# Performance work log

Measured on AMD Instinct MI355X. Metric: run time of the kernel, lower is better.

The kernel has to match this reference:

```python
import jax, jax.numpy as jnp
import numpy as np

KSIZE = 3
KN = (KSIZE - 1) // 2  # 1
TEMP = 50.0


def _extract_patches(x, same_pad):
    """TF tf.image.extract_patches ordering: per location, (dy, dx, channel).
    x: [b,H,W,d] -> [b,h,w,9*d] (h=H,w=W if same_pad else H-2,W-2)."""
    if same_pad:
        x = jnp.pad(x, ((0, 0), (KN, KN), (KN, KN), (0, 0)))
    b, Hp, Wp, d = x.shape
    h, w = Hp - 2 * KN, Wp - 2 * KN
    slices = [x[:, dy:dy + h, dx:dx + w, :]
              for dy in range(KSIZE) for dx in range(KSIZE)]
    return jnp.concatenate(slices, axis=-1)


def setup_inputs() -> dict:
    key = jax.random.key(0)
    k1, k2, k3 = jax.random.split(key, 3)
    b, h, w, dims = 4, 48, 48, 64
    g_in = jax.random.normal(k1, (b, h, w, dims), dtype=jnp.float32)
    # binary inpainting mask (1 = known background, 0 = hole)
    mask = (jax.random.uniform(k2, (b, h, w, 1)) > 0.5).astype(jnp.float32)
    W2 = jax.random.normal(k3, (2 * dims, dims), dtype=jnp.float32) / np.sqrt(2.0 * dims)
    b2 = jnp.zeros((dims,), dtype=jnp.float32)
    return {"g_in": g_in, "mask": mask, "W2": W2, "b2": b2}


def reference(g_in, mask, W2, b2):
    b, h, w, dims = g_in.shape
    c = (h - 2 * KN) * (w - 2 * KN)

    mask_r = mask  # already (h,w,1); broadcasts over dims (== tile)
    bg = g_in * mask_r

    # p1: VALID 3x3 patches of bg -> dynamic kernels, [b, c, 9*dims]
    p1 = _extract_patches(bg, same_pad=False).reshape(b, c, KSIZE * KSIZE * dims)
    # p2: SAME 3x3 patches of g_in, [b, h, w, 9*dims]
    p2 = _extract_patches(g_in, same_pad=True)

    # cross-correlation: conv2d(ft, k1) == per-location dot with each bg patch
    CS = jnp.einsum('byxk,bjk->byxj', p2, p1)              # [b,h,w,c]
    k1d = jnp.sum(p1 * p1, axis=2)                          # [b,c]
    wwd = jnp.sum(p2 * p2, axis=3, keepdims=True)           # [b,h,w,1]
    DS1 = k1d[:, None, None, :] + wwd - 2.0 * CS            # squared distances
    mu = jnp.mean(DS1, axis=3, keepdims=True)
    sd = jnp.std(DS1, axis=3, keepdims=True)                # population std (tf.math.reduce_std)
    DS2 = -jnp.tanh((DS1 - mu) / sd)
    CA = jax.nn.softmax(TEMP * DS2, axis=-1)                # [b,h,w,c]

    # transposed conv aggregation with per-sample kernels k2[b,j,dy,dx,ch]
    k2 = p1.reshape(b, c, KSIZE, KSIZE, dims)
    CA_pad = jnp.pad(CA, ((0, 0), (KN, KN), (KN, KN), (0, 0)))
    acl = jnp.zeros((b, h, w, dims), dtype=g_in.dtype)
    for dy in range(KSIZE):
        for dx in range(KSIZE):
            win = CA_pad[:, 2 * KN - dy:2 * KN - dy + h, 2 * KN - dx:2 * KN - dx + w, :]
            acl = acl + jnp.einsum('byxj,bjd->byxd', win, k2[:, :, dy, dx, :])
    acl = acl / 9.0

    ACL = bg + acl * (1.0 - mask_r)
    con1 = jnp.concatenate([g_in, ACL], axis=3)             # [b,h,w,2*dims]
    return jax.nn.elu(jnp.einsum('byxk,kd->byxd', con1, W2) + b2)
```

## Files before the change

kernel.cpp:

```cpp
#include <hip/hip_runtime.h>
#include <hip/hip_fp16.h>
#include <math.h>

#define BB 4
#define HH 48
#define WW 48
#define DD 64
#define CC 2116
#define HWp (HH*WW)
#define PW 50
#define PP (PW*PW)

#define SLOTW 48
#define NSLOT 2208
#define NGRP 276
#define KSPLIT0 1120
#define QW 2304
#define QROWS 2500

typedef __attribute__((ext_vector_type(8))) short short8;
typedef __attribute__((ext_vector_type(8))) _Float16 half8;
typedef __attribute__((ext_vector_type(4))) float float4v;

#define OFFB_GPAD  ((size_t)0)
#define OFFB_BGPAD ((size_t)1280000)
#define OFFB_E     ((size_t)2560000)
#define OFFB_K1D   ((size_t)2596864)
#define OFFB_BGT3  ((size_t)2632192)
#define OFFB_F     ((size_t)6023680)
#define OFFB_CA    ((size_t)52103680)
#define OFFB_CAY   ((size_t)92801536)
#define OFFB_ACLP  ((size_t)133499392)

__device__ __forceinline__ ushort f2bf(float x) {
    unsigned u = __float_as_uint(x);
    return (ushort)((u + 0x7FFFu + ((u >> 16) & 1u)) >> 16);
}

__device__ __forceinline__ float waveReduceSum(float x) {
#pragma unroll
    for (int o = 32; o > 0; o >>= 1) x += __shfl_down(x, o, 64);
    return x;
}

__device__ __forceinline__ __half2 u2h2(uint u) {
    union { uint u; __half2 h; } c; c.u = u; return c.h;
}

__device__ __forceinline__ uint cvtpk_bf16(float lo, float hi) {
    uint r;
    asm("v_cvt_pk_bf16_f32 %0, %1, %2" : "=v"(r) : "v"(lo), "v"(hi));
    return r;
}

__device__ __forceinline__ float softexp(float d, float mu, float isd) {
    float z = (d - mu) * isd;
    float E2 = __expf(z + z);
    float r = __builtin_amdgcn_rcpf(E2 + 1.f);
    return __expf(fmaf(100.f, r, -50.f));
}

typedef __attribute__((address_space(3))) void lds_void_t;
typedef __attribute__((address_space(1))) void gmem_void_t;
__device__ __forceinline__ void gld16(const ushort* g, ushort* lds) {
    __builtin_amdgcn_global_load_lds((gmem_void_t*)g, (lds_void_t*)lds, 16, 0, 0);
}

__global__ __launch_bounds__(256) void build_pads(const float* __restrict__ g,
                                                  const float* __restrict__ mask,
                                                  ushort* __restrict__ gpad,
                                                  ushort* __restrict__ bgpad,
                                                  float* __restrict__ e) {
    int w = threadIdx.x >> 6, c = threadIdx.x & 63;
    int q4 = blockIdx.x * 4 + w;
    int b = q4 / PP, q = q4 % PP;
    int yp = q / PW, xp = q % PW;
    size_t o = (size_t)q4 * DD + c;
    if (yp >= 1 && yp <= HH && xp >= 1 && xp <= WW) {
        int pix = (yp - 1) * WW + (xp - 1);
        float gv = g[((size_t)b * HWp + pix) * DD + c];
        float m  = mask[(size_t)b * HWp + pix];
        float bgv = gv * m;
        gpad[o]  = f2bf(gv);
        bgpad[o] = f2bf(bgv);
        float ss = waveReduceSum(bgv * bgv);
        if (c == 0) e[b * HWp + pix] = ss;
    } else {
        gpad[o] = 0;
        bgpad[o] = 0;
    }
}

__global__ __launch_bounds__(256) void build_bgt3_k1d(const ushort* __restrict__ bgpad,
                                                      const float* __restrict__ e,
                                                      ushort* __restrict__ bgT3,
                                                      float* __restrict__ k1d) {
    int b = blockIdx.y;
    int t = threadIdx.x;
    if (blockIdx.x == 35) {
#pragma unroll 1
        for (int st = t; st < NSLOT; st += 256) {
            int jy = st / SLOTW, jx = st - jy * SLOTW;
            float s = 0.f;
            if (jx < 46) {
                const float* eb = e + (size_t)b * HWp + jy * WW + jx;
#pragma unroll
                for (int ddy = 0; ddy < 3; ddy++)
#pragma unroll
                    for (int ddx = 0; ddx < 3; ddx++) s += eb[ddy * WW + ddx];
            }
            k1d[(size_t)b * NSLOT + st] = s;
        }
        return;
    }
    __shared__ ushort T[66 * 65];
    int jt = blockIdx.x;
    const ushort* src = bgpad + (size_t)b * PP * DD;
    int lr = t >> 3, c8 = (t & 7) * 8;
#pragma unroll
    for (int pass = 0; pass < 2; pass++) {
        int r = lr + pass * 32;
        int v = jt * 64 + r;
        int vy = v / 48, vx = v - vy * 48;
        uint4 d = *(const uint4*)(src + (size_t)((vy + 1) * PW + (vx + 1)) * DD + c8);
        ushort tmp[8];
        *(uint4*)tmp = d;
#pragma unroll
        for (int u = 0; u < 8; u++) {
            float f = __uint_as_float((uint)tmp[u] << 16);
            __half h = __float2half_rn(f);
            T[r * 65 + c8 + u] = *(ushort*)&h;
        }
    }
    if (t < 16) {
        int r = 64 + (t >> 3);
        int c8b = (t & 7) * 8;
        int v = jt * 64 + r;
        int vy = v / 48, vx = v - vy * 48;
        uint4 d = *(const uint4*)(src + (size_t)((vy + 1) * PW + (vx + 1)) * DD + c8b);
        ushort tmp[8];
        *(uint4*)tmp = d;
#pragma unroll
        for (int u = 0; u < 8; u++) {
            float f = __uint_as_float((uint)tmp[u] << 16);
            __half h = __float2half_rn(f);
            T[r * 65 + c8b + u] = *(ushort*)&h;
        }
    }
    __syncthreads();
#pragma unroll
    for (int pass = 0; pass < 2; pass++) {
        int c = lr + pass * 32;
        int j8 = (t & 7) * 8;
        int col0 = jt * 64 + j8;
        if (col0 < NSLOT) {
#pragma unroll
            for (int dx = 0; dx < 3; dx++) {
                ushort tmp[8];
#pragma unroll
                for (int u = 0; u < 8; u++) tmp[u] = T[(j8 + u + dx) * 65 + c];
                *(uint4*)(bgT3 + ((size_t)b * 192 + dx * 64 + c) * NSLOT + col0) =
                    *(const uint4*)tmp;
            }
        }
    }
}

__global__ __launch_bounds__(256) void fgemm(const ushort* __restrict__ gpad,
                                             const ushort* __restrict__ bgpad,
                                             __half* __restrict__ Fout) {
    __shared__ ushort As[2 * 4096];
    __shared__ ushort Bs[2 * 4096];
    int i0 = blockIdx.x;
    int b = (i0 & 7) >> 1;
    int tile = ((i0 >> 3) << 1) | (i0 & 1);
    int ty = tile / 18, tx = tile - ty * 18;
    int m0 = ty * 128, n0 = tx * 128;
    const ushort* Ag = gpad + (size_t)b * PP * DD;
    const ushort* Bg = bgpad + (size_t)b * PP * DD;

    int tid = threadIdx.x;
    int l = tid & 63, w = tid >> 6;
    int quad = l >> 4, l15 = l & 15;
    int sw8 = (l15 >> 1) & 3;
    int wm = (w >> 1) * 64, wn = (w & 1) * 64;
    int rowInC = l >> 2;
    int cSw = (l & 3) ^ ((l >> 3) & 3);

    int baseA[2], baseB[2];
#pragma unroll
    for (int i = 0; i < 2; i++) {
        int rg = w * 2 + i;
        int r = rg * 16 + rowInC;
        int u = m0 + r; if (u > QROWS - 1) u = QROWS - 1;
        int n = n0 + r;
        int vy = n / 48, vx = n - vy * 48;
        baseA[i] = u * DD + cSw * 8;
        baseB[i] = ((vy + 1) * PW + (vx + 1)) * DD + cSw * 8;
    }

    float4v acc[4][4];
#pragma unroll
    for (int i = 0; i < 4; i++)
#pragma unroll
        for (int j = 0; j < 4; j++) acc[i][j] = (float4v){0.f, 0.f, 0.f, 0.f};

#pragma unroll
    for (int i = 0; i < 2; i++) {
        int rg = w * 2 + i;
        gld16(Ag + baseA[i], As + rg * 512);
        gld16(Bg + baseB[i], Bs + rg * 512);
    }

    int buf = 0;
    for (int k0 = 0; k0 < 192; k0 += 32) {
        __syncthreads();
        int nb = buf ^ 1;
        if (k0 + 32 < 192) {
#pragma unroll
            for (int i = 0; i < 2; i++) {
                int rg = w * 2 + i;
                gld16(Ag + baseA[i] + (k0 + 32), As + nb * 4096 + rg * 512);
                gld16(Bg + baseB[i] + (k0 + 32), Bs + nb * 4096 + rg * 512);
            }
        }
        const ushort* Ax = As + buf * 4096;
        const ushort* Bx = Bs + buf * 4096;
        short8 af[4], bf[4];
#pragma unroll
        for (int i = 0; i < 4; i++)
            af[i] = *(const short8*)&Ax[(wm + i * 16 + l15) * 32 + ((quad ^ sw8)) * 8];
#pragma unroll
        for (int j = 0; j < 4; j++)
            bf[j] = *(const short8*)&Bx[(wn + j * 16 + l15) * 32 + ((quad ^ sw8)) * 8];
#pragma unroll
        for (int i = 0; i < 4; i++)
#pragma unroll
            for (int j = 0; j < 4; j++)
                acc[i][j] = __builtin_amdgcn_mfma_f32_16x16x32_bf16(af[i], bf[j], acc[i][j], 0, 0, 0);
        buf = nb;
    }

    __half* C = Fout + (size_t)b * QROWS * QW;
#pragma unroll
    for (int i = 0; i < 4; i++) {
#pragma unroll
        for (int j = 0; j < 4; j++) {
            int n = n0 + wn + j * 16 + l15;
#pragma unroll
            for (int r = 0; r < 4; r++) {
                int m = m0 + wm + i * 16 + quad * 4 + r;
                if (m < QROWS) C[(size_t)m * QW + n] = __float2half(acc[i][j][r]);
            }
        }
    }
}

__global__ __launch_bounds__(320) void qrowsoft4(const __half* __restrict__ F,
                                                 const float* __restrict__ k1d,
                                                 ushort* __restrict__ CA) {
    __shared__ float red[8][321];
    int i0 = blockIdx.x;
    int b = (i0 & 7) >> 1;
    int sub = ((i0 >> 3) << 1) | (i0 & 1);
    int y = sub / 12, xt = sub - y * 12;
    int x0 = xt * 4;

    int t = threadIdx.x;
    bool act = (t < NGRP);
    int jy = t / 6, jxb = (t - jy * 6) * 8;
    int slot0 = jy * SLOTW + jxb;
    bool vc6 = act && (jxb == 40);

    __half2 acc[4][4];
#pragma unroll
    for (int p = 0; p < 4; p++)
#pragma unroll
        for (int k = 0; k < 4; k++) acc[p][k] = u2h2(0u);

    float k1v[8] = {0.f, 0.f, 0.f, 0.f, 0.f, 0.f, 0.f, 0.f};

    if (act) {
        const float* k1 = k1d + (size_t)b * NSLOT + slot0;
        float4 ka = *(const float4*)k1;
        float4 kb = *(const float4*)(k1 + 4);
        k1v[0] = ka.x; k1v[1] = ka.y; k1v[2] = ka.z; k1v[3] = ka.w;
        k1v[4] = kb.x; k1v[5] = kb.y; k1v[6] = kb.z; k1v[7] = kb.w;

#pragma unroll
        for (int dy = 0; dy < 3; dy++) {
            const __half* R = F + ((size_t)b * QROWS + (size_t)(y + dy) * PW + x0) * QW
                            + slot0 + dy * 48;
#pragma unroll
            for (int p = 0; p < 4; p++) {
                uint4 v4 = *(const uint4*)(R + (size_t)p * QW);
                acc[p][0] = __hadd2(acc[p][0], u2h2(v4.x));
                acc[p][1] = __hadd2(acc[p][1], u2h2(v4.y));
                acc[p][2] = __hadd2(acc[p][2], u2h2(v4.z));
                acc[p][3] = __hadd2(acc[p][3], u2h2(v4.w));
            }
        }
    }

    if (vc6) {
#pragma unroll
        for (int p = 0; p < 4; p++) acc[p][3] = u2h2(0u);
    }

#pragma unroll
    for (int p = 0; p < 4; p++) {
        float s1p = 0.f, s2p = 0.f;
#pragma unroll
        for (int k = 0; k < 4; k++) {
            float2 f = __half22float2(acc[p][k]);
            float d0 = k1v[2*k]   - 2.f * f.x;
            float d1 = k1v[2*k+1] - 2.f * f.y;
            s1p += d0 + d1;
            s2p = fmaf(d0, d0, fmaf(d1, d1, s2p));
        }
        red[p][t] = s1p;
        red[4 + p][t] = s2p;
    }
    __syncthreads();
    if (t < 128) {
        int v = t >> 4, sb = t & 15;
        float s = 0.f;
#pragma unroll
        for (int k = 0; k < 20; k++) s += red[v][sb + 16 * k];
#pragma unroll
        for (int o = 8; o > 0; o >>= 1) s += __shfl_down(s, o, 16);
        if (sb == 0) red[v][320] = s;
    }
    __syncthreads();
    float mu[4], isd[4];
#pragma unroll
    for (int p = 0; p < 4; p++) {
        float m = red[p][320] * (1.f / (float)CC);
        float ex2 = red[4 + p][320] * (1.f / (float)CC);
        mu[p] = m;
        isd[p] = rsqrtf(ex2 - m * m);
    }

    uint eb[4][4];
#pragma unroll
    for (int p = 0; p < 4; p++) {
        float es = 0.f;
#pragma unroll
        for (int k = 0; k < 4; k++) {
            float2 f = __half22float2(acc[p][k]);
            float d0 = k1v[2*k]   - 2.f * f.x;
            float d1 = k1v[2*k+1] - 2.f * f.y;
            if (k == 3 && vc6) { d0 = 1e9f; d1 = 1e9f; }
            float e0 = softexp(d0, mu[p], isd[p]);
            float e1 = softexp(d1, mu[p], isd[p]);
            es += e0 + e1;
            eb[p][k] = cvtpk_bf16(e0, e1);
        }
        red[p][t] = act ? es : 0.f;
    }
    __syncthreads();
    if (t < 64) {
        int v = t >> 4, sb = t & 15;
        float s = 0.f;
#pragma unroll
        for (int k = 0; k < 20; k++) s += red[v][sb + 16 * k];
#pragma unroll
        for (int o = 8; o > 0; o >>= 1) s += __shfl_down(s, o, 16);
        if (sb == 0) red[v][320] = s;
    }
    __syncthreads();

    if (act) {
#pragma unroll
        for (int p = 0; p < 4; p++) {
            float iz = __builtin_amdgcn_rcpf(red[p][320]);
            uint o[4];
#pragma unroll
            for (int k = 0; k < 4; k++) {
                uint wv = eb[p][k];
                float lo = __uint_as_float(wv << 16) * iz;
                float hi = __uint_as_float(wv & 0xffff0000u) * iz;
                __half2 hh = __halves2half2(__float2half_rn(lo), __float2half_rn(hi));
                o[k] = *(uint*)&hh;
            }
            int pix = y * WW + x0 + p;
            ushort* wp = CA + ((size_t)b * HWp + pix) * (size_t)NSLOT + slot0;
            *(uint4*)wp = *(const uint4*)o;
        }
    }
}

__global__ __launch_bounds__(320) void cay_k(const ushort* __restrict__ CAu,
                                             ushort* __restrict__ CAy) {
    int i0 = blockIdx.x;
    int b = (i0 & 7) >> 1;
    int sub = ((i0 >> 3) << 1) | (i0 & 1);
    int y = sub / 12, xt = sub - y * 12;
    int x0 = xt * 4;

    int t = threadIdx.x;
    if (t >= NGRP) return;
    int jy = t / 6, jxb = (t - jy * 6) * 8;
    int slot0 = jy * SLOTW + jxb;

    __half2 acc[4][4];
#pragma unroll
    for (int p = 0; p < 4; p++)
#pragma unroll
        for (int k = 0; k < 4; k++) acc[p][k] = u2h2(0u);

#pragma unroll
    for (int dy = 0; dy < 3; dy++) {
        int yy = y + 1 - dy;
        if (yy < 0 || yy >= 48) continue;
        if (jy < dy) continue;
        const ushort* rp = CAu + ((size_t)b * HWp + yy * 48 + x0) * (size_t)NSLOT
                         + slot0 - 48 * dy;
#pragma unroll
        for (int p = 0; p < 4; p++) {
            uint4 v4 = *(const uint4*)(rp + (size_t)p * NSLOT);
            acc[p][0] = __hadd2(acc[p][0], u2h2(v4.x));
            acc[p][1] = __hadd2(acc[p][1], u2h2(v4.y));
            acc[p][2] = __hadd2(acc[p][2], u2h2(v4.z));
            acc[p][3] = __hadd2(acc[p][3], u2h2(v4.w));
        }
    }

#pragma unroll
    for (int p = 0; p < 4; p++) {
        uint o[4];
#pragma unroll
        for (int k = 0; k < 4; k++) {
            __half2 h = acc[p][k];
            o[k] = *(uint*)&h;
        }
        *(uint4*)(CAy + ((size_t)b * HWp + y * 48 + x0 + p) * (size_t)NSLOT + slot0) =
            *(const uint4*)o;
    }
}

__global__ __launch_bounds__(256) void gemm4(const ushort* __restrict__ Am,
                                             const ushort* __restrict__ Bm,
                                             float* __restrict__ aclp) {
    __shared__ ushort As[2 * 4096];
    __shared__ ushort Bs[2 * 2048];
    int i0 = blockIdx.x;
    int z = i0 & 7;
    int b = z >> 1, s = z & 1;
    int tile = i0 >> 3;
    int ty = tile / 3, tx = tile - ty * 3;
    int m0 = ty * 128, n0 = tx * 64;
    int kb = s ? KSPLIT0 : 0;
    int ke = s ? NSLOT : KSPLIT0;
    const ushort* Ab = Am + ((size_t)b * HWp + m0) * (size_t)NSLOT;
    const ushort* Bb = Bm + ((size_t)b * 192 + n0) * (size_t)NSLOT;

    int tid = threadIdx.x;
    int l = tid & 63, w = tid >> 6;
    int quad = l >> 4, l15 = l & 15;
    int sw8 = (l15 >> 1) & 3;
    int wm = w * 32;
    int rowInC = l >> 2;
    int cSw = (l & 3) ^ ((l >> 3) & 3);

    float4v acc[2][4];
#pragma unroll
    for (int i = 0; i < 2; i++)
#pragma unroll
        for (int j = 0; j < 4; j++) acc[i][j] = (float4v){0.f, 0.f, 0.f, 0.f};

#pragma unroll
    for (int i = 0; i < 2; i++) {
        int rg = w * 2 + i;
        gld16(Ab + (size_t)(rg * 16 + rowInC) * NSLOT + kb + cSw * 8, As + rg * 512);
    }
    gld16(Bb + (size_t)(w * 16 + rowInC) * NSLOT + kb + cSw * 8, Bs + w * 512);

    int buf = 0;
    for (int k0 = kb; k0 < ke; k0 += 32) {
        __syncthreads();
        int nb = buf ^ 1;
        if (k0 + 32 < ke) {
#pragma unroll
            for (int i = 0; i < 2; i++) {
                int rg = w * 2 + i;
                gld16(Ab + (size_t)(rg * 16 + rowInC) * NSLOT + (k0 + 32) + cSw * 8,
                      As + nb * 4096 + rg * 512);
            }
            gld16(Bb + (size_t)(w * 16 + rowInC) * NSLOT + (k0 + 32) + cSw * 8,
                  Bs + nb * 2048 + w * 512);
        }
        const ushort* Ax = As + buf * 4096;
        const ushort* Bx = Bs + buf * 2048;
        half8 af[2], bf[4];
#pragma unroll
        for (int i = 0; i < 2; i++)
            af[i] = *(const half8*)&Ax[(wm + i * 16 + l15) * 32 + ((quad ^ sw8)) * 8];
#pragma unroll
        for (int j = 0; j < 4; j++)
            bf[j] = *(const half8*)&Bx[(j * 16 + l15) * 32 + ((quad ^ sw8)) * 8];
#pragma unroll
        for (int i = 0; i < 2; i++)
#pragma unroll
            for (int j = 0; j < 4; j++)
                acc[i][j] = __builtin_amdgcn_mfma_f32_16x16x32_f16(af[i], bf[j], acc[i][j], 0, 0, 0);
        buf = nb;
    }

    float* C = aclp + ((size_t)s * (BB * HWp) + (size_t)b * HWp) * 192;
#pragma unroll
    for (int i = 0; i < 2; i++)
#pragma unroll
        for (int j = 0; j < 4; j++)
#pragma unroll
            for (int r = 0; r < 4; r++) {
                int m = m0 + wm + i * 16 + quad * 4 + r;
                int n = n0 + j * 16 + l15;
                C[(size_t)m * 192 + n] = acc[i][j][r];
            }
}

__global__ __launch_bounds__(256) void final_k3(const float* __restrict__ g,
                                                const float* __restrict__ mask,
                                                const float* __restrict__ aclp,
                                                const float* __restrict__ W2,
                                                const float* __restrict__ b2,
                                                float* __restrict__ out) {
    int w = threadIdx.x >> 6, d = threadIdx.x & 63;
    int pix = blockIdx.x * 4 + w;
    int b = pix / HWp, yx = pix % HWp;
    int y = yx / WW, x = yx % WW;

    __shared__ float con1[4][128];
    float acl = 0.f;
#pragma unroll
    for (int dx = 0; dx < 3; dx++) {
        int xs = x + 1 - dx;
        if (xs >= 0 && xs < WW) {
            size_t off = ((size_t)b * HWp + y * WW + xs) * 192 + dx * 64 + d;
            acl += aclp[off] + aclp[off + (size_t)BB * HWp * 192];
        }
    }

    float m = mask[pix];
    float gv = g[(size_t)pix * DD + d];
    float bgv = gv * m;
    float ACL = bgv + (acl / 9.f) * (1.f - m);
    con1[w][d] = gv;
    con1[w][64 + d] = ACL;
    __syncthreads();
    float accv = b2[d];
#pragma unroll 8
    for (int k = 0; k < 128; k++) accv = fmaf(con1[w][k], W2[k * 64 + d], accv);
    out[(size_t)pix * DD + d] = accv > 0.f ? accv : expm1f(accv);
}

extern "C" void kernel_launch(void* const* d_in, const int* in_sizes, int n_in,
                              void* d_out, int out_size, void* d_ws, size_t ws_size,
                              hipStream_t stream) {
    const float* g    = (const float*)d_in[0];
    const float* mask = (const float*)d_in[1];
    const float* W2   = (const float*)d_in[2];
    const float* b2   = (const float*)d_in[3];
    float* out = (float*)d_out;
    char* ws = (char*)d_ws;

    ushort* gpad  = (ushort*)(ws + OFFB_GPAD);
    ushort* bgpad = (ushort*)(ws + OFFB_BGPAD);
    float*  e     = (float*) (ws + OFFB_E);
    float*  k1d   = (float*) (ws + OFFB_K1D);
    ushort* bgT3  = (ushort*)(ws + OFFB_BGT3);
    __half* Fbuf  = (__half*)(ws + OFFB_F);
    ushort* CA    = (ushort*)(ws + OFFB_CA);
    ushort* CAy   = (ushort*)(ws + OFFB_CAY);
    float*  aclp  = (float*) (ws + OFFB_ACLP);

    build_pads<<<BB * PP / 4, 256, 0, stream>>>(g, mask, gpad, bgpad, e);
    build_bgt3_k1d<<<dim3(36, BB), 256, 0, stream>>>(bgpad, e, bgT3, k1d);

    fgemm<<<1440, 256, 0, stream>>>(gpad, bgpad, Fbuf);
    qrowsoft4<<<BB * HWp / 4, 320, 0, stream>>>(Fbuf, k1d, CA);

    cay_k<<<BB * HWp / 4, 320, 0, stream>>>(CA, CAy);
    gemm4<<<432, 256, 0, stream>>>(CAy, bgT3, aclp);

    final_k3<<<BB * HWp / 4, 256, 0, stream>>>(g, mask, aclp, W2, b2, out);
}
```

Before: 169.6 us.

## Fuse vertical CA shift-sum into aggregation GEMM and retile with 4-way K split

```diff
diff --git a/kernel.cpp b/kernel.cpp
--- a/kernel.cpp
+++ b/kernel.cpp
@@ -14,7 +14,6 @@
 #define SLOTW 48
 #define NSLOT 2208
 #define NGRP 276
-#define KSPLIT0 1120
 #define QW 2304
 #define QROWS 2500
 
@@ -29,8 +28,7 @@
 #define OFFB_BGT3  ((size_t)2632192)
 #define OFFB_F     ((size_t)6023680)
 #define OFFB_CA    ((size_t)52103680)
-#define OFFB_CAY   ((size_t)92801536)
-#define OFFB_ACLP  ((size_t)133499392)
+#define OFFB_ACLP  ((size_t)92801536)
 
 __device__ __forceinline__ ushort f2bf(float x) {
     unsigned u = __float_as_uint(x);
@@ -45,6 +43,9 @@
 
 __device__ __forceinline__ __half2 u2h2(uint u) {
     union { uint u; __half2 h; } c; c.u = u; return c.h;
+}
+__device__ __forceinline__ uint h2u(__half2 h) {
+    union { __half2 h; uint u; } c; c.h = h; return c.u;
 }
 
 __device__ __forceinline__ uint cvtpk_bf16(float lo, float hi) {
@@ -256,15 +257,15 @@
     }
 }
 
-__global__ __launch_bounds__(320) void qrowsoft4(const __half* __restrict__ F,
+__global__ __launch_bounds__(320) void qrowsoft5(const __half* __restrict__ F,
                                                  const float* __restrict__ k1d,
                                                  ushort* __restrict__ CA) {
     __shared__ float red[8][321];
     int i0 = blockIdx.x;
     int b = (i0 & 7) >> 1;
     int sub = ((i0 >> 3) << 1) | (i0 & 1);
-    int y = sub / 12, xt = sub - y * 12;
-    int x0 = xt * 4;
+    int yq = sub / 48, x = sub - yq * 48;
+    int y0 = yq * 4;
 
     int t = threadIdx.x;
     bool act = (t < NGRP);
@@ -287,17 +288,20 @@
         k1v[0] = ka.x; k1v[1] = ka.y; k1v[2] = ka.z; k1v[3] = ka.w;
         k1v[4] = kb.x; k1v[5] = kb.y; k1v[6] = kb.z; k1v[7] = kb.w;
 
-#pragma unroll
-        for (int dy = 0; dy < 3; dy++) {
-            const __half* R = F + ((size_t)b * QROWS + (size_t)(y + dy) * PW + x0) * QW
-                            + slot0 + dy * 48;
-#pragma unroll
-            for (int p = 0; p < 4; p++) {
-                uint4 v4 = *(const uint4*)(R + (size_t)p * QW);
-                acc[p][0] = __hadd2(acc[p][0], u2h2(v4.x));
-                acc[p][1] = __hadd2(acc[p][1], u2h2(v4.y));
-                acc[p][2] = __hadd2(acc[p][2], u2h2(v4.z));
-                acc[p][3] = __hadd2(acc[p][3], u2h2(v4.w));
+        const __half* Fb = F + ((size_t)b * QROWS + (size_t)y0 * PW + x) * QW + slot0;
+#pragma unroll
+        for (int r = 0; r < 6; r++) {
+            const __half* R = Fb + (size_t)r * PW * QW;
+#pragma unroll
+            for (int dy = 0; dy < 3; dy++) {
+                int p = r - dy;
+                if (p >= 0 && p < 4) {
+                    uint4 v4 = *(const uint4*)(R + 48 * dy);
+                    acc[p][0] = __hadd2(acc[p][0], u2h2(v4.x));
+                    acc[p][1] = __hadd2(acc[p][1], u2h2(v4.y));
+                    acc[p][2] = __hadd2(acc[p][2], u2h2(v4.z));
+                    acc[p][3] = __hadd2(acc[p][3], u2h2(v4.w));
+                }
             }
         }
     }
@@ -383,144 +387,134 @@
                 __half2 hh = __halves2half2(__float2half_rn(lo), __float2half_rn(hi));
                 o[k] = *(uint*)&hh;
             }
-            int pix = y * WW + x0 + p;
+            int pix = (y0 + p) * WW + x;
             ushort* wp = CA + ((size_t)b * HWp + pix) * (size_t)NSLOT + slot0;
             *(uint4*)wp = *(const uint4*)o;
         }
     }
 }
 
-__global__ __launch_bounds__(320) void cay_k(const ushort* __restrict__ CAu,
-                                             ushort* __restrict__ CAy) {
+__device__ __forceinline__ uint4 loadA3(const ushort* __restrict__ CAu,
+                                        const int* base3, int v0) {
+    int jy = v0 / 48;
+    __half2 a0 = u2h2(0u), a1 = u2h2(0u), a2 = u2h2(0u), a3 = u2h2(0u);
+#pragma unroll
+    for (int dy = 0; dy < 3; dy++) {
+        if (base3[dy] >= 0 && jy >= dy) {
+            uint4 v = *(const uint4*)(CAu + base3[dy] + v0 - 48 * dy);
+            a0 = __hadd2(a0, u2h2(v.x)); a1 = __hadd2(a1, u2h2(v.y));
+            a2 = __hadd2(a2, u2h2(v.z)); a3 = __hadd2(a3, u2h2(v.w));
+        }
+    }
+    uint4 r;
+    r.x = h2u(a0); r.y = h2u(a1); r.z = h2u(a2); r.w = h2u(a3);
+    return r;
+}
+
+__global__ __launch_bounds__(256) void gemm4f(const ushort* __restrict__ CAu,
+                                              const ushort* __restrict__ Bm,
+                                              float* __restrict__ aclp) {
+    __shared__ ushort As[2 * 4096];
+    __shared__ ushort Bs[2 * 6144];
     int i0 = blockIdx.x;
     int b = (i0 & 7) >> 1;
-    int sub = ((i0 >> 3) << 1) | (i0 & 1);
-    int y = sub / 12, xt = sub - y * 12;
-    int x0 = xt * 4;
-
-    int t = threadIdx.x;
-    if (t >= NGRP) return;
-    int jy = t / 6, jxb = (t - jy * 6) * 8;
-    int slot0 = jy * SLOTW + jxb;
-
-    __half2 acc[4][4];
-#pragma unroll
-    for (int p = 0; p < 4; p++)
-#pragma unroll
-        for (int k = 0; k < 4; k++) acc[p][k] = u2h2(0u);
-
-#pragma unroll
-    for (int dy = 0; dy < 3; dy++) {
-        int yy = y + 1 - dy;
-        if (yy < 0 || yy >= 48) continue;
-        if (jy < dy) continue;
-        const ushort* rp = CAu + ((size_t)b * HWp + yy * 48 + x0) * (size_t)NSLOT
-                         + slot0 - 48 * dy;
-#pragma unroll
-        for (int p = 0; p < 4; p++) {
-            uint4 v4 = *(const uint4*)(rp + (size_t)p * NSLOT);
-            acc[p][0] = __hadd2(acc[p][0], u2h2(v4.x));
-            acc[p][1] = __hadd2(acc[p][1], u2h2(v4.y));
-            acc[p][2] = __hadd2(acc[p][2], u2h2(v4.z));
-            acc[p][3] = __hadd2(acc[p][3], u2h2(v4.w));
-        }
-    }
-
-#pragma unroll
-    for (int p = 0; p < 4; p++) {
-        uint o[4];
-#pragma unroll
-        for (int k = 0; k < 4; k++) {
-            __half2 h = acc[p][k];
-            o[k] = *(uint*)&h;
-        }
-        *(uint4*)(CAy + ((size_t)b * HWp + y * 48 + x0 + p) * (size_t)NSLOT + slot0) =
-            *(const uint4*)o;
-    }
-}
-
-__global__ __launch_bounds__(256) void gemm4(const ushort* __restrict__ Am,
-                                             const ushort* __restrict__ Bm,
-                                             float* __restrict__ aclp) {
-    __shared__ ushort As[2 * 4096];
-    __shared__ ushort Bs[2 * 2048];
-    int i0 = blockIdx.x;
-    int z = i0 & 7;
-    int b = z >> 1, s = z & 1;
-    int tile = i0 >> 3;
-    int ty = tile / 3, tx = tile - ty * 3;
-    int m0 = ty * 128, n0 = tx * 64;
-    int kb = s ? KSPLIT0 : 0;
-    int ke = s ? NSLOT : KSPLIT0;
-    const ushort* Ab = Am + ((size_t)b * HWp + m0) * (size_t)NSLOT;
-    const ushort* Bb = Bm + ((size_t)b * 192 + n0) * (size_t)NSLOT;
+    int t2 = ((i0 >> 3) << 1) | (i0 & 1);
+    int s = t2 & 3, mt = t2 >> 2;
+    int m0 = mt * 128;
+    const int KB0[5] = {0, 576, 1120, 1664, 2208};
+    int kb = KB0[s], ke = KB0[s + 1];
 
     int tid = threadIdx.x;
     int l = tid & 63, w = tid >> 6;
     int quad = l >> 4, l15 = l & 15;
     int sw8 = (l15 >> 1) & 3;
-    int wm = w * 32;
+    int wm = (w >> 1) * 64, wn = (w & 1) * 96;
     int rowInC = l >> 2;
     int cSw = (l & 3) ^ ((l >> 3) & 3);
-
-    float4v acc[2][4];
-#pragma unroll
-    for (int i = 0; i < 2; i++)
-#pragma unroll
-        for (int j = 0; j < 4; j++) acc[i][j] = (float4v){0.f, 0.f, 0.f, 0.f};
-
+    int cS8 = cSw * 8;
+
+    int baseA[2][3];
 #pragma unroll
     for (int i = 0; i < 2; i++) {
-        int rg = w * 2 + i;
-        gld16(Ab + (size_t)(rg * 16 + rowInC) * NSLOT + kb + cSw * 8, As + rg * 512);
-    }
-    gld16(Bb + (size_t)(w * 16 + rowInC) * NSLOT + kb + cSw * 8, Bs + w * 512);
+        int m = m0 + (w * 2 + i) * 16 + rowInC;
+        int y = m / 48, x = m - y * 48;
+#pragma unroll
+        for (int dy = 0; dy < 3; dy++) {
+            int yy = y + 1 - dy;
+            baseA[i][dy] = (yy >= 0 && yy < 48)
+                         ? (int)(((size_t)b * HWp + yy * 48 + x) * NSLOT) : -1;
+        }
+    }
+    const ushort* Bb = Bm + (size_t)b * 192 * (size_t)NSLOT;
+
+    float4v acc[4][6];
+#pragma unroll
+    for (int i = 0; i < 4; i++)
+#pragma unroll
+        for (int j = 0; j < 6; j++) acc[i][j] = (float4v){0.f, 0.f, 0.f, 0.f};
+
+    uint4 rA[2];
+#pragma unroll
+    for (int i = 0; i < 2; i++) rA[i] = loadA3(CAu, baseA[i], kb + cS8);
+#pragma unroll
+    for (int i = 0; i < 2; i++) *(uint4*)&As[(w * 2 + i) * 512 + l * 8] = rA[i];
+#pragma unroll
+    for (int i = 0; i < 3; i++) {
+        int rg = w * 3 + i;
+        gld16(Bb + (size_t)(rg * 16 + rowInC) * NSLOT + kb + cS8, Bs + rg * 512);
+    }
 
     int buf = 0;
     for (int k0 = kb; k0 < ke; k0 += 32) {
         __syncthreads();
         int nb = buf ^ 1;
-        if (k0 + 32 < ke) {
-#pragma unroll
-            for (int i = 0; i < 2; i++) {
-                int rg = w * 2 + i;
-                gld16(Ab + (size_t)(rg * 16 + rowInC) * NSLOT + (k0 + 32) + cSw * 8,
-                      As + nb * 4096 + rg * 512);
-            }
-            gld16(Bb + (size_t)(w * 16 + rowInC) * NSLOT + (k0 + 32) + cSw * 8,
-                  Bs + nb * 2048 + w * 512);
+        bool hasNext = (k0 + 32 < ke);
+        if (hasNext) {
+#pragma unroll
+            for (int i = 0; i < 2; i++) rA[i] = loadA3(CAu, baseA[i], (k0 + 32) + cS8);
+#pragma unroll
+            for (int i = 0; i < 3; i++) {
+                int rg = w * 3 + i;
+                gld16(Bb + (size_t)(rg * 16 + rowInC) * NSLOT + (k0 + 32) + cS8,
+                      Bs + nb * 6144 + rg * 512);
+            }
         }
         const ushort* Ax = As + buf * 4096;
-        const ushort* Bx = Bs + buf * 2048;
-        half8 af[2], bf[4];
-#pragma unroll
-        for (int i = 0; i < 2; i++)
+        const ushort* Bx = Bs + buf * 6144;
+        half8 af[4], bf[6];
+#pragma unroll
+        for (int i = 0; i < 4; i++)
             af[i] = *(const half8*)&Ax[(wm + i * 16 + l15) * 32 + ((quad ^ sw8)) * 8];
 #pragma unroll
-        for (int j = 0; j < 4; j++)
-            bf[j] = *(const half8*)&Bx[(j * 16 + l15) * 32 + ((quad ^ sw8)) * 8];
-#pragma unroll
-        for (int i = 0; i < 2; i++)
-#pragma unroll
-            for (int j = 0; j < 4; j++)
+        for (int j = 0; j < 6; j++)
+            bf[j] = *(const half8*)&Bx[(wn + j * 16 + l15) * 32 + ((quad ^ sw8)) * 8];
+#pragma unroll
+        for (int i = 0; i < 4; i++)
+#pragma unroll
+            for (int j = 0; j < 6; j++)
                 acc[i][j] = __builtin_amdgcn_mfma_f32_16x16x32_f16(af[i], bf[j], acc[i][j], 0, 0, 0);
+        if (hasNext) {
+#pragma unroll
+            for (int i = 0; i < 2; i++)
+                *(uint4*)&As[nb * 4096 + (w * 2 + i) * 512 + l * 8] = rA[i];
+        }
         buf = nb;
     }
 
     float* C = aclp + ((size_t)s * (BB * HWp) + (size_t)b * HWp) * 192;
 #pragma unroll
-    for (int i = 0; i < 2; i++)
-#pragma unroll
-        for (int j = 0; j < 4; j++)
+    for (int i = 0; i < 4; i++)
+#pragma unroll
+        for (int j = 0; j < 6; j++)
 #pragma unroll
             for (int r = 0; r < 4; r++) {
                 int m = m0 + wm + i * 16 + quad * 4 + r;
-                int n = n0 + j * 16 + l15;
+                int n = wn + j * 16 + l15;
                 C[(size_t)m * 192 + n] = acc[i][j][r];
             }
 }
 
-__global__ __launch_bounds__(256) void final_k3(const float* __restrict__ g,
+__global__ __launch_bounds__(256) void final_k4(const float* __restrict__ g,
                                                 const float* __restrict__ mask,
                                                 const float* __restrict__ aclp,
                                                 const float* __restrict__ W2,
@@ -538,7 +532,9 @@
         int xs = x + 1 - dx;
         if (xs >= 0 && xs < WW) {
             size_t off = ((size_t)b * HWp + y * WW + xs) * 192 + dx * 64 + d;
-            acl += aclp[off] + aclp[off + (size_t)BB * HWp * 192];
+#pragma unroll
+            for (int s = 0; s < 4; s++)
+                acl += aclp[off + (size_t)s * (BB * HWp) * 192];
         }
     }
 
@@ -572,17 +568,15 @@
     ushort* bgT3  = (ushort*)(ws + OFFB_BGT3);
     __half* Fbuf  = (__half*)(ws + OFFB_F);
     ushort* CA    = (ushort*)(ws + OFFB_CA);
-    ushort* CAy   = (ushort*)(ws + OFFB_CAY);
     float*  aclp  = (float*) (ws + OFFB_ACLP);
 
     build_pads<<<BB * PP / 4, 256, 0, stream>>>(g, mask, gpad, bgpad, e);
     build_bgt3_k1d<<<dim3(36, BB), 256, 0, stream>>>(bgpad, e, bgT3, k1d);
 
     fgemm<<<1440, 256, 0, stream>>>(gpad, bgpad, Fbuf);
-    qrowsoft4<<<BB * HWp / 4, 320, 0, stream>>>(Fbuf, k1d, CA);
-
-    cay_k<<<BB * HWp / 4, 320, 0, stream>>>(CA, CAy);
-    gemm4<<<432, 256, 0, stream>>>(CAy, bgT3, aclp);
-
-    final_k3<<<BB * HWp / 4, 256, 0, stream>>>(g, mask, aclp, W2, b2, out);
-}
+    qrowsoft5<<<BB * HWp / 4, 320, 0, stream>>>(Fbuf, k1d, CA);
+
+    gemm4f<<<288, 256, 0, stream>>>(CA, bgT3, aclp);
+
+    final_k4<<<BB * HWp / 4, 256, 0, stream>>>(g, mask, aclp, W2, b2, out);
+}
```

New measurement: 226.9 us. +33.8%, slower.
